# Optimization experiments

Hardware: AMD Instinct MI355X
Metric: run time of the kernel (lower is better)

Reference implementation:

```python
import jax, jax.numpy as jnp
import numpy as np

N_NODES = 100000
N_EDGES = 2000000
N_BASIS = 32
CUTOFF = 5.0


def setup_inputs() -> dict:
    key = jax.random.key(0)
    k1, k2, k3 = jax.random.split(key, 3)
    coordinates = jax.random.normal(k1, (N_NODES, 3), dtype=jnp.float32) * 10.0
    receivers = jax.random.randint(k2, (1, N_EDGES), 0, N_NODES, dtype=jnp.int64)
    senders = jax.random.randint(k3, (1, N_EDGES), 0, N_NODES, dtype=jnp.int64)
    # learned (here frozen) RBF parameters, exactly as in __init__
    mu = jnp.asarray(
        np.linspace(np.exp(-CUTOFF), 1.0, num=N_BASIS, dtype=np.float32).reshape(1, N_BASIS)
    )
    beta = jnp.full(
        (1, N_BASIS), (2.0 / N_BASIS * (1.0 - np.exp(-CUTOFF))) ** (-2), dtype=jnp.float32
    )
    return {"coordinates": coordinates, "receivers": receivers, "senders": senders,
            "mu": mu, "beta": beta}


def reference(coordinates, receivers, senders, mu, beta):
    # gather endpoint coords: [B, E, 3]
    recv_xyz = coordinates[receivers]
    send_xyz = coordinates[senders]
    # pairwise distance, flattened to [B*E, 1]
    r_ij = jnp.sqrt(jnp.sum(jnp.square(recv_xyz - send_xyz), axis=2))
    r_ij = r_ij.reshape(-1, 1)
    # polynomial cutoff function phi(r)
    u = r_ij / CUTOFF
    phi = 1.0 - 6.0 * u ** 5 + 15.0 * u ** 4 - 10.0 * u ** 3
    # Gaussian RBF in exp(-r) space, modulated by cutoff: [B*E, n_basis]
    rbf = jnp.exp(-beta * jnp.square(jnp.exp(-r_ij) - mu)) * phi
    return rbf
```

## Files before the change

kernel.cpp:

```cpp
#include <hip/hip_runtime.h>

#define CUTOFF 5.0f
#define NB 32

typedef float f32x4 __attribute__((ext_vector_type(4)));

__global__ __launch_bounds__(256) void physnet_rbf_kernel(
    const float* __restrict__ coords,
    const int*   __restrict__ recv,
    const int*   __restrict__ send,
    const float* __restrict__ mu,
    const float* __restrict__ beta,
    float*       __restrict__ out,
    int n_edges)
{
    int t    = blockIdx.x * blockDim.x + threadIdx.x;
    int lane = threadIdx.x & 63;
    int ebase = (t >> 6) * 8;

    float er = 0.0f, phi = 0.0f;
    if (lane < 8) {
        int e = ebase + lane;
        if (e < n_edges) {
            int ir = recv[e];
            int is = send[e];
            const float* cr = coords + (size_t)ir * 3;
            const float* cs = coords + (size_t)is * 3;
            float dx = cr[0] - cs[0];
            float dy = cr[1] - cs[1];
            float dz = cr[2] - cs[2];
            float r  = sqrtf(dx * dx + dy * dy + dz * dz);
            float u  = r * (1.0f / CUTOFF);
            float u3 = u * u * u;
            phi = 1.0f + u3 * (-10.0f + u * (15.0f - 6.0f * u));
            er  = __expf(-r);
        }
    }
    int sub = lane >> 3;
    er  = __shfl(er,  sub);
    phi = __shfl(phi, sub);

    int e = ebase + sub;
    if (e >= n_edges) return;

    int k4 = (lane & 7) << 2;
    float4 m = *reinterpret_cast<const float4*>(mu + k4);
    float4 b = *reinterpret_cast<const float4*>(beta + k4);

    f32x4 o;
    float d0 = er - m.x; o.x = __expf(-b.x * d0 * d0) * phi;
    float d1 = er - m.y; o.y = __expf(-b.y * d1 * d1) * phi;
    float d2 = er - m.z; o.z = __expf(-b.z * d2 * d2) * phi;
    float d3 = er - m.w; o.w = __expf(-b.w * d3 * d3) * phi;

    __builtin_nontemporal_store(o, reinterpret_cast<f32x4*>(out + (size_t)e * NB + k4));
}

extern "C" void kernel_launch(void* const* d_in, const int* in_sizes, int n_in,
                              void* d_out, int out_size, void* d_ws, size_t ws_size,
                              hipStream_t stream) {
    const float* coords = (const float*)d_in[0];
    const int*   recv   = (const int*)d_in[1];
    const int*   send   = (const int*)d_in[2];
    const float* mu     = (const float*)d_in[3];
    const float* beta   = (const float*)d_in[4];
    float*       out    = (float*)d_out;

    int n_edges = in_sizes[1];
    long long n_threads = (long long)n_edges * 8;
    int block = 256;
    long long grid = (n_threads + block - 1) / block;

    physnet_rbf_kernel<<<(int)grid, block, 0, stream>>>(coords, recv, send, mu, beta,
                                                        out, n_edges);
}
```

Measured before the change: 51.37 us.

## Compute per-edge distance once per lane and loop over 64 edges per wave

Each wave now handles 64 edges. Every lane computes the distance, cutoff and exp(-r) for one edge, where before only 8 of 64 lanes did this work. The wave then loops 8 times, using shuffles to broadcast each edge's values so every lane writes a float4 slice of the 32-wide RBF output. This removes the idle lanes in the gather phase and cuts the grid size by 8x. The cost is longer-running threads with a serialized store loop, which gives fewer waves in flight to hide memory latency.

Measured after the change: 54.25 us. 5.6% more time.

```diff
diff --git a/kernel.cpp b/kernel.cpp
--- a/kernel.cpp
+++ b/kernel.cpp
@@ -14,46 +14,48 @@
     float*       __restrict__ out,
     int n_edges)
 {
-    int t    = blockIdx.x * blockDim.x + threadIdx.x;
-    int lane = threadIdx.x & 63;
-    int ebase = (t >> 6) * 8;
+    int lane  = threadIdx.x & 63;
+    int wid   = blockIdx.x * (blockDim.x >> 6) + (threadIdx.x >> 6);
+    int ebase = wid * 64;
 
     float er = 0.0f, phi = 0.0f;
-    if (lane < 8) {
-        int e = ebase + lane;
-        if (e < n_edges) {
-            int ir = recv[e];
-            int is = send[e];
-            const float* cr = coords + (size_t)ir * 3;
-            const float* cs = coords + (size_t)is * 3;
-            float dx = cr[0] - cs[0];
-            float dy = cr[1] - cs[1];
-            float dz = cr[2] - cs[2];
-            float r  = sqrtf(dx * dx + dy * dy + dz * dz);
-            float u  = r * (1.0f / CUTOFF);
-            float u3 = u * u * u;
-            phi = 1.0f + u3 * (-10.0f + u * (15.0f - 6.0f * u));
-            er  = __expf(-r);
-        }
+    int e = ebase + lane;
+    if (e < n_edges) {
+        int ir = recv[e];
+        int is = send[e];
+        const float* cr = coords + (size_t)ir * 3;
+        const float* cs = coords + (size_t)is * 3;
+        float dx = cr[0] - cs[0];
+        float dy = cr[1] - cs[1];
+        float dz = cr[2] - cs[2];
+        float r  = sqrtf(dx * dx + dy * dy + dz * dz);
+        float u  = r * (1.0f / CUTOFF);
+        float u3 = u * u * u;
+        phi = 1.0f + u3 * (-10.0f + u * (15.0f - 6.0f * u));
+        er  = __expf(-r);
     }
-    int sub = lane >> 3;
-    er  = __shfl(er,  sub);
-    phi = __shfl(phi, sub);
-
-    int e = ebase + sub;
-    if (e >= n_edges) return;
 
     int k4 = (lane & 7) << 2;
     float4 m = *reinterpret_cast<const float4*>(mu + k4);
     float4 b = *reinterpret_cast<const float4*>(beta + k4);
+    int sub = lane >> 3;
 
-    f32x4 o;
-    float d0 = er - m.x; o.x = __expf(-b.x * d0 * d0) * phi;
-    float d1 = er - m.y; o.y = __expf(-b.y * d1 * d1) * phi;
-    float d2 = er - m.z; o.z = __expf(-b.z * d2 * d2) * phi;
-    float d3 = er - m.w; o.w = __expf(-b.w * d3 * d3) * phi;
-
-    __builtin_nontemporal_store(o, reinterpret_cast<f32x4*>(out + (size_t)e * NB + k4));
+    #pragma unroll
+    for (int i = 0; i < 8; ++i) {
+        int src = i * 8 + sub;
+        float er_i  = __shfl(er,  src);
+        float phi_i = __shfl(phi, src);
+        int eo = ebase + src;
+        if (eo < n_edges) {
+            f32x4 o;
+            float d0 = er_i - m.x; o.x = __expf(-b.x * d0 * d0) * phi_i;
+            float d1 = er_i - m.y; o.y = __expf(-b.y * d1 * d1) * phi_i;
+            float d2 = er_i - m.z; o.z = __expf(-b.z * d2 * d2) * phi_i;
+            float d3 = er_i - m.w; o.w = __expf(-b.w * d3 * d3) * phi_i;
+            __builtin_nontemporal_store(
+                o, reinterpret_cast<f32x4*>(out + (size_t)eo * NB + k4));
+        }
+    }
 }
 
 extern "C" void kernel_launch(void* const* d_in, const int* in_sizes, int n_in,
@@ -67,10 +69,9 @@
     float*       out    = (float*)d_out;
 
     int n_edges = in_sizes[1];
-    long long n_threads = (long long)n_edges * 8;
     int block = 256;
-    long long grid = (n_threads + block - 1) / block;
+    int grid = (n_edges + block - 1) / block;
 
-    physnet_rbf_kernel<<<(int)grid, block, 0, stream>>>(coords, recv, send, mu, beta,
-                                                        out, n_edges);
+    physnet_rbf_kernel<<<grid, block, 0, stream>>>(coords, recv, send, mu, beta,
+                                                   out, n_edges);
 }
```
